# Kernel tuning notes

Hardware: AMD Instinct MI355X
Metric: run time of the kernel (lower is better)

The kernel has to match this reference:

```python
import jax, jax.numpy as jnp
import numpy as np
import math

B, NIN, DIM, QK, GS, L, BINS = 512, 128, 512, 128, 32, 2, 100
HID = int(DIM * 2.0)
G = NIN // GS
ROT = 32  # rotary dim = min(32, query_key_dim)
EPS = 1e-5


def setup_inputs() -> dict:
    key = jax.random.key(0)
    ks = jax.random.split(key, 8)
    r = jax.random.normal
    return {
        "tokens": jax.random.randint(ks[0], (B, NIN), 0, BINS),
        "emb": r(ks[1], (NIN, BINS, DIM), jnp.float32) * 0.02,
        "pos_emb": r(ks[2], (NIN, DIM), jnp.float32) * 0.01,
        "norm_g": jnp.ones((L,), jnp.float32),
        "Wh": r(ks[3], (L, DIM, 2 * HID), jnp.float32) / math.sqrt(DIM),
        "bh": jnp.zeros((L, 2 * HID), jnp.float32),
        "Wqk": r(ks[4], (L, DIM, QK), jnp.float32) / math.sqrt(DIM),
        "bqk": jnp.zeros((L, QK), jnp.float32),
        "gamma": r(ks[5], (L, 4, QK), jnp.float32) * 0.02,
        "beta": jnp.zeros((L, 4, QK), jnp.float32),
        "rp": r(ks[6], (L, 32), jnp.float32) * 0.02,
        "Wout": r(ks[7], (L, HID, DIM), jnp.float32) / math.sqrt(HID),
        "bout": jnp.zeros((L, DIM), jnp.float32),
        "ln_g": jnp.ones((DIM,), jnp.float32),
        "ln_b": jnp.zeros((DIM,), jnp.float32),
    }


def _t5_buckets(n, num_buckets=32, max_distance=128):
    # causal T5 relative position buckets, computed statically
    pos = np.arange(n)
    rel = pos[None, :] - pos[:, None]
    neg = np.maximum(-rel, 0)
    max_exact = num_buckets // 2
    vl = max_exact + (np.log(np.maximum(neg, 1) / max_exact) / np.log(max_distance / max_exact) * (num_buckets - max_exact)).astype(np.int64)
    vl = np.minimum(vl, num_buckets - 1)
    return jnp.asarray(np.where(neg < max_exact, neg, vl))


def _rotary_cos_sin(n):
    inv = 1.0 / (10000.0 ** (np.arange(0, ROT, 2) / ROT))
    f = np.einsum('i,j->ij', np.arange(n), inv)  # [n, ROT/2]
    f = np.repeat(f, 2, axis=-1)                 # interleaved-pair freqs [n, ROT]
    return jnp.asarray(np.cos(f), jnp.float32), jnp.asarray(np.sin(f), jnp.float32)


def _apply_rotary(x, cos, sin):
    xr, xp = x[..., :ROT], x[..., ROT:]
    x2 = xr.reshape(*xr.shape[:-1], ROT // 2, 2)
    rh = jnp.stack((-x2[..., 1], x2[..., 0]), axis=-1).reshape(xr.shape)
    return jnp.concatenate([xr * cos + rh * sin, xp], axis=-1)


def reference(tokens, emb, pos_emb, norm_g, Wh, bh, Wqk, bqk, gamma, beta, rp, Wout, bout, ln_g, ln_b):
    # per-column embedding lookup + positional embedding
    x = emb[jnp.arange(NIN)[None, :], tokens] + pos_emb  # [B, NIN, DIM]
    buckets = _t5_buckets(GS)
    cos, sin = _rotary_cos_sin(NIN)
    t5_scale = QK ** 0.5
    causal_mask = jnp.triu(jnp.ones((GS, GS), bool), 1)

    def grp(t):
        return t.reshape(B, G, GS, t.shape[-1])

    def layer(h, p):
        ng, Wh_l, bh_l, Wqk_l, bqk_l, gm, bt, rp_l, Wo_l, bo_l = p
        # ScaleNorm
        nrm = jnp.linalg.norm(h, axis=-1, keepdims=True) * DIM ** -0.5
        nx = h / jnp.maximum(nrm, EPS) * ng
        # shift_tokens: shift first half of features by one position
        xs, xp = nx[..., :DIM // 2], nx[..., DIM // 2:]
        xs = jnp.pad(xs, ((0, 0), (1, 0), (0, 0)))[:, :-1]
        nx = jnp.concatenate([xs, xp], axis=-1)
        hid = jax.nn.silu(nx @ Wh_l + bh_l)
        v, gate = hid[..., :HID], hid[..., HID:]
        qk = jax.nn.silu(nx @ Wqk_l + bqk_l)
        qs = qk[..., None, :] * gm + bt  # [B, NIN, 4, QK]
        quad_q = _apply_rotary(qs[..., 0, :], cos, sin)
        lin_q = _apply_rotary(qs[..., 1, :], cos, sin)
        quad_k = _apply_rotary(qs[..., 2, :], cos, sin)
        lin_k = _apply_rotary(qs[..., 3, :], cos, sin)
        qq, lq, kk, lk, vg = map(grp, (quad_q, lin_q, quad_k, lin_k, v))
        # grouped quadratic attention with ReLU^2 attn fn and T5 rel-pos bias
        sim = jnp.einsum('bgid,bgjd->bgij', qq, kk) / GS + rp_l[buckets] * t5_scale
        attn = jnp.square(jax.nn.relu(sim))
        attn = jnp.where(causal_mask, 0.0, attn)
        quad_out = jnp.einsum('bgij,bgje->bgie', attn, vg)
        # causal linear attention across groups (shifted cumsum of kv stats)
        lin_kv = jnp.einsum('bgnd,bgne->bgde', lk, vg) / GS
        lin_kv = jnp.cumsum(lin_kv, axis=1)
        lin_kv = jnp.pad(lin_kv, ((0, 0), (1, 0), (0, 0), (0, 0)))[:, :-1]
        lin_out = jnp.einsum('bgde,bgnd->bgne', lin_kv, lq)
        out = gate * (quad_out + lin_out).reshape(B, NIN, HID)
        return out @ Wo_l + bo_l + h, None

    x, _ = jax.lax.scan(layer, x, (norm_g, Wh, bh, Wqk, bqk, gamma, beta, rp, Wout, bout))
    mu = x.mean(-1, keepdims=True)
    var = x.var(-1, keepdims=True)
    return (x - mu) / jnp.sqrt(var + EPS) * ln_g + ln_b
```

## Files before the change

### kernel.cpp

```cpp
#include <hip/hip_runtime.h>
#include <hip/hip_bf16.h>
#include <math.h>
#include <stdint.h>

#define BB   512
#define NIN  128
#define DIMD 512
#define QKD  128
#define GSZ  32
#define GRP  4
#define HID  1024
#define HID2 2048
#define NFUSE 2176
#define ROT  32
#define NLAYER 2
#define EPSF 1e-5f
#define BINS 100

typedef __bf16 bf16x8 __attribute__((ext_vector_type(8)));
typedef float  f32x4  __attribute__((ext_vector_type(4)));
typedef float  f32x16 __attribute__((ext_vector_type(16)));

__device__ __forceinline__ unsigned short f2bf(float f) {
    union { float f; uint32_t u; } v; v.f = f;
    return (unsigned short)((v.u + 0x7FFFu + ((v.u >> 16) & 1u)) >> 16);
}
__device__ __forceinline__ float bf2f(unsigned short h) {
    union { uint32_t u; float f; } v; v.u = ((uint32_t)h) << 16;
    return v.f;
}

__global__ void k_embed(const int* __restrict__ tokens, const float* __restrict__ emb,
                        const float* __restrict__ pos, float* __restrict__ h) {
    int bn = blockIdx.x;
    int n  = bn % NIN;
    int tok = tokens[bn];
    const float4* e4 = (const float4*)(emb + ((size_t)n * BINS + tok) * DIMD);
    const float4* p4 = (const float4*)(pos + (size_t)n * DIMD);
    float4* h4 = (float4*)(h + (size_t)bn * DIMD);
    int t = threadIdx.x;
    float4 a = e4[t], b = p4[t];
    h4[t] = make_float4(a.x + b.x, a.y + b.y, a.z + b.z, a.w + b.w);
}

__global__ void k_rms(const float* __restrict__ h, float* __restrict__ scale,
                      const float* __restrict__ ngp) {
    int row  = blockIdx.x * 4 + (threadIdx.x >> 6);
    int lane = threadIdx.x & 63;
    const float4* r4 = (const float4*)(h + (size_t)row * DIMD);
    float s = 0.f;
    #pragma unroll
    for (int i = 0; i < 2; ++i) {
        float4 v = r4[lane + 64 * i];
        s += v.x * v.x + v.y * v.y + v.z * v.z + v.w * v.w;
    }
    #pragma unroll
    for (int o = 32; o; o >>= 1) s += __shfl_down(s, o);
    if (lane == 0) {
        float nrm = sqrtf(s) * (1.0f / sqrtf((float)DIMD));
        scale[row] = ngp[0] / fmaxf(nrm, EPSF);
    }
}

__global__ void k_nx(const float* __restrict__ h, const float* __restrict__ scale,
                     unsigned short* __restrict__ nx) {
    int bn = blockIdx.x; int n = bn % NIN;
    int t = threadIdx.x;
    float4 v; float sc;
    if (t < 64) {
        if (n == 0) {
            ((ushort4*)(nx + (size_t)bn * DIMD))[t] = make_ushort4(0, 0, 0, 0);
            return;
        }
        sc = scale[bn - 1];
        v = ((const float4*)(h + (size_t)(bn - 1) * DIMD))[t];
    } else {
        sc = scale[bn];
        v = ((const float4*)(h + (size_t)bn * DIMD))[t];
    }
    ushort4 o = make_ushort4(f2bf(v.x * sc), f2bf(v.y * sc), f2bf(v.z * sc), f2bf(v.w * sc));
    ((ushort4*)(nx + (size_t)bn * DIMD))[t] = o;
}

__global__ void k_wcast(const float* __restrict__ W, unsigned short* __restrict__ Wt,
                        int K, int N) {
    int idx = blockIdx.x * 256 + threadIdx.x;
    int total = N * (K / 8);
    if (idx >= total) return;
    int kb = idx / N, n = idx % N;
    #pragma unroll
    for (int j = 0; j < 8; ++j)
        Wt[(size_t)n * K + kb * 8 + j] = f2bf(W[(size_t)(kb * 8 + j) * N + n]);
}

#define GLOAD_LDS(gp, lp) __builtin_amdgcn_global_load_lds( \
    (const __attribute__((address_space(1))) uint32_t*)(gp), \
    (__attribute__((address_space(3))) uint32_t*)(lp), 16, 0, 0)

template<int MODE>
__global__ __launch_bounds__(256, 2) void k_gemm2(
        const unsigned short* __restrict__ A,
        const unsigned short* __restrict__ Bt,
        const float* __restrict__ bias0,
        const float* __restrict__ bias1,
        const float* __restrict__ resid,
        float* __restrict__ Cf,
        unsigned short* __restrict__ vTp,
        unsigned short* __restrict__ gatep,
        int M, int N, int K) {
    __shared__ unsigned short As[2][256 * 32];
    __shared__ unsigned short Bs[2][128 * 32];
    const int tid = threadIdx.x;

    int flat = blockIdx.y * gridDim.x + blockIdx.x;
    int nwg  = gridDim.x * gridDim.y;
    int q = nwg >> 3, r = nwg & 7;
    int xcd = flat & 7, idx = flat >> 3;
    int swz = (xcd < r ? xcd * (q + 1) : r * (q + 1) + (xcd - r) * q) + idx;
    const int bxi = swz % gridDim.x, byi = swz / gridDim.x;
    const int bm = byi * 256, bn = bxi * 128;

    const int lane = tid & 63, wave = tid >> 6;
    const int l15 = lane & 15, l4 = lane >> 4;

    f32x4 acc[4][8];
    #pragma unroll
    for (int i = 0; i < 4; ++i)
        #pragma unroll
        for (int j = 0; j < 8; ++j) acc[i][j] = (f32x4){0.f, 0.f, 0.f, 0.f};

    const int rowA = tid >> 2;
    const int colO = (tid & 3) * 16;
    const int colS = colO ^ ((rowA & 3) << 4);
    const char* gA = (const char*)(A  + (size_t)(bm + rowA) * K) + colS;
    const char* gB = (const char*)(Bt + (size_t)(bn + rowA) * K) + colS;
    const size_t stride64 = (size_t)64 * K * 2;
    unsigned short* dA0 = &As[0][tid * 8];
    unsigned short* dA1 = &As[1][tid * 8];
    unsigned short* dB0 = &Bs[0][tid * 8];
    unsigned short* dB1 = &Bs[1][tid * 8];

    #define STAGE2(dA, dB, k0) do { \
        const char* sA_ = gA + (size_t)(k0) * 2; \
        const char* sB_ = gB + (size_t)(k0) * 2; \
        GLOAD_LDS(sA_,                 (dA)); \
        GLOAD_LDS(sA_ +     stride64,  (dA) + 2048); \
        GLOAD_LDS(sA_ + 2 * stride64,  (dA) + 4096); \
        GLOAD_LDS(sA_ + 3 * stride64,  (dA) + 6144); \
        GLOAD_LDS(sB_,                 (dB)); \
        GLOAD_LDS(sB_ +     stride64,  (dB) + 2048); \
    } while (0)

    STAGE2(dA0, dB0, 0);
    asm volatile("s_waitcnt vmcnt(0)" ::: "memory");
    __syncthreads();

    const int NIT = K / 32;
    int bufc = 0;
    for (int it = 0; it < NIT; ++it) {
        if (it + 1 < NIT) {
            if (bufc == 0) STAGE2(dA1, dB1, (it + 1) * 32);
            else           STAGE2(dA0, dB0, (it + 1) * 32);
        }
        const unsigned short* Ab = As[bufc];
        const unsigned short* Bb = Bs[bufc];
        bf16x8 af[4], bfr[8];
        #pragma unroll
        for (int f = 0; f < 4; ++f) {
            int rA = wave * 64 + f * 16 + l15;
            af[f] = *(const bf16x8*)&Ab[rA * 32 + ((l4 ^ (rA & 3)) << 3)];
        }
        #pragma unroll
        for (int c = 0; c < 8; ++c) {
            int rB = c * 16 + l15;
            bfr[c] = *(const bf16x8*)&Bb[rB * 32 + ((l4 ^ (rB & 3)) << 3)];
        }
        #pragma unroll
        for (int f = 0; f < 4; ++f)
            #pragma unroll
            for (int c = 0; c < 8; ++c)
                acc[f][c] = __builtin_amdgcn_mfma_f32_16x16x32_bf16(af[f], bfr[c], acc[f][c], 0, 0, 0);
        asm volatile("s_waitcnt vmcnt(0)" ::: "memory");
        __syncthreads();
        bufc ^= 1;
    }
    #undef STAGE2

    #pragma unroll
    for (int f = 0; f < 4; ++f) {
        const int n0 = wave * 64 + f * 16 + l4 * 4;
        #pragma unroll
        for (int c = 0; c < 8; ++c) {
            const int col = bn + c * 16 + l15;
            if (MODE == 0) {
                float bsv = (col < 2 * HID) ? bias0[col] : bias1[col - 2 * HID];
                float vv[4];
                #pragma unroll
                for (int rr = 0; rr < 4; ++rr) {
                    float v = acc[f][c][rr] + bsv;
                    vv[rr] = v / (1.0f + __expf(-v));
                }
                if (col < HID) {
                    size_t batch = (size_t)byi * 2 + (n0 >> 7);
                    ushort4 o = make_ushort4(f2bf(vv[0]), f2bf(vv[1]), f2bf(vv[2]), f2bf(vv[3]));
                    *(ushort4*)&vTp[(batch * HID + col) * NIN + (n0 & 127)] = o;
                } else if (col < 2 * HID) {
                    #pragma unroll
                    for (int rr = 0; rr < 4; ++rr)
                        gatep[(size_t)(bm + n0 + rr) * HID + (col - HID)] = f2bf(vv[rr]);
                } else {
                    #pragma unroll
                    for (int rr = 0; rr < 4; ++rr)
                        Cf[(size_t)(bm + n0 + rr) * QKD + (col - 2 * HID)] = vv[rr];
                }
            } else {
                float bsv = bias0[col];
                #pragma unroll
                for (int rr = 0; rr < 4; ++rr) {
                    size_t row = bm + n0 + rr;
                    Cf[row * N + col] = acc[f][c][rr] + bsv + resid[row * N + col];
                }
            }
        }
    }
}

__global__ void k_cossin(float* __restrict__ cosb, float* __restrict__ sinb) {
    int idx = blockIdx.x * 256 + threadIdx.x;
    if (idx >= NIN * 16) return;
    int n = idx / 16, i = idx % 16;
    double inv = pow(10000.0, -(double)(2 * i) / (double)ROT);
    double f = (double)n * inv;
    cosb[idx] = (float)cos(f);
    sinb[idx] = (float)sin(f);
}

__global__ void k_rot(const float* __restrict__ qk, const float* __restrict__ gm,
                      const float* __restrict__ bt, const float* __restrict__ cosb,
                      const float* __restrict__ sinb, unsigned short* __restrict__ q4) {
    int bn = blockIdx.x; int n = bn % NIN;
    int d = threadIdx.x;
    float x = qk[(size_t)bn * QKD + d];
    float xp0 = 0.f;
    int dp = d ^ 1;
    if (d < ROT) xp0 = qk[(size_t)bn * QKD + dp];
    #pragma unroll
    for (int c = 0; c < 4; ++c) {
        float val = x * gm[c * QKD + d] + bt[c * QKD + d];
        float outv;
        if (d < ROT) {
            int i = d >> 1;
            float cs = cosb[n * 16 + i], sn = sinb[n * 16 + i];
            float xp = xp0 * gm[c * QKD + dp] + bt[c * QKD + dp];
            outv = ((d & 1) == 0) ? (val * cs - xp * sn) : (val * cs + xp * sn);
        } else outv = val;
        q4[((size_t)bn * 4 + c) * QKD + d] = f2bf(outv);
    }
}

__global__ __launch_bounds__(256) void k_attn2(
        const unsigned short* __restrict__ q4,
        const unsigned short* __restrict__ gatep,
        const unsigned short* __restrict__ vT,
        const float* __restrict__ rp,
        unsigned short* __restrict__ attn_out) {
    int et = blockIdx.x, b = blockIdx.y;
    int tid = threadIdx.x, wave = tid >> 6, lane = tid & 63;
    int l31 = lane & 31, lhi = lane >> 5;

    __shared__ unsigned short S[32][136];
    __shared__ float rps_d[32];
    if (tid < 32) {
        int d = tid, bucket;
        if (d < 16) bucket = d;
        else {
            bucket = 16 + (int)(logf((float)d * (1.0f / 16.0f)) * (16.0f / logf(8.0f)));
            if (bucket > 31) bucket = 31;
        }
        rps_d[tid] = rp[bucket] * sqrtf((float)QKD);
    }
    __syncthreads();

    size_t bbase = (size_t)b * NIN;
    int e0 = et * 256 + wave * 64;
    const unsigned short* vbase = vT + (size_t)b * HID * NIN;

    for (int g = 0; g < GRP; ++g) {
        if (wave <= g) {
            int gp = wave;
            bool quad = (gp == g);
            const unsigned short* Qb = q4 + ((bbase + g  * 32 + l31) * 4 + (quad ? 0 : 1)) * QKD;
            const unsigned short* Kb = q4 + ((bbase + gp * 32 + l31) * 4 + (quad ? 2 : 3)) * QKD;
            f32x16 sa = {};
            #pragma unroll
            for (int kk = 0; kk < 8; ++kk) {
                bf16x8 aq = *(const bf16x8*)(Qb + kk * 16 + lhi * 8);
                bf16x8 bk = *(const bf16x8*)(Kb + kk * 16 + lhi * 8);
                sa = __builtin_amdgcn_mfma_f32_32x32x16_bf16(aq, bk, sa, 0, 0, 0);
            }
            int j = l31;
            #pragma unroll
            for (int r = 0; r < 16; ++r) {
                int i = (r & 3) + 8 * (r >> 2) + 4 * lhi;
                float s = sa[r] * (1.0f / GSZ);
                if (quad) {
                    if (j > i) s = 0.f;
                    else {
                        s += rps_d[i - j];
                        s = fmaxf(s, 0.f);
                        s = s * s;
                    }
                }
                S[i][gp * 32 + j] = f2bf(s);
            }
        }
        __syncthreads();

        f32x16 o0 = {}, o1 = {};
        int KT = 2 * (g + 1);
        for (int kk = 0; kk < KT; ++kk) {
            int k0 = kk * 16 + lhi * 8;
            bf16x8 af = *(const bf16x8*)&S[l31][k0];
            bf16x8 b0 = *(const bf16x8*)(vbase + (size_t)(e0 + l31) * NIN + k0);
            bf16x8 b1 = *(const bf16x8*)(vbase + (size_t)(e0 + 32 + l31) * NIN + k0);
            o0 = __builtin_amdgcn_mfma_f32_32x32x16_bf16(af, b0, o0, 0, 0, 0);
            o1 = __builtin_amdgcn_mfma_f32_32x32x16_bf16(af, b1, o1, 0, 0, 0);
        }
        __syncthreads();

        int ea = e0 + l31, eb = e0 + 32 + l31;
        #pragma unroll
        for (int r = 0; r < 16; ++r) {
            int i = (r & 3) + 8 * (r >> 2) + 4 * lhi;
            size_t row = bbase + g * 32 + i;
            float ga = bf2f(gatep[row * HID + ea]);
            float gb = bf2f(gatep[row * HID + eb]);
            attn_out[row * HID + ea] = f2bf(ga * o0[r]);
            attn_out[row * HID + eb] = f2bf(gb * o1[r]);
        }
    }
}

__global__ void k_ln(const float* __restrict__ h, const float* __restrict__ lng,
                     const float* __restrict__ lnb, float* __restrict__ out) {
    int bn = blockIdx.x;
    int t = threadIdx.x;
    const float4* r4 = (const float4*)(h + (size_t)bn * DIMD);
    float4 v = r4[t];
    float s  = v.x + v.y + v.z + v.w;
    float sq = v.x * v.x + v.y * v.y + v.z * v.z + v.w * v.w;
    __shared__ float red[4];
    #pragma unroll
    for (int o = 32; o; o >>= 1) { s += __shfl_down(s, o); sq += __shfl_down(sq, o); }
    int lane = t & 63, w = t >> 6;
    if (lane == 0) { red[w] = s; red[2 + w] = sq; }
    __syncthreads();
    float mu  = (red[0] + red[1]) * (1.0f / DIMD);
    float var = (red[2] + red[3]) * (1.0f / DIMD) - mu * mu;
    float rstd = 1.0f / sqrtf(var + EPSF);
    float4 gg = ((const float4*)lng)[t];
    float4 bb = ((const float4*)lnb)[t];
    float4 o;
    o.x = (v.x - mu) * rstd * gg.x + bb.x;
    o.y = (v.y - mu) * rstd * gg.y + bb.y;
    o.z = (v.z - mu) * rstd * gg.z + bb.z;
    o.w = (v.w - mu) * rstd * gg.w + bb.w;
    ((float4*)(out + (size_t)bn * DIMD))[t] = o;
}

extern "C" void kernel_launch(void* const* d_in, const int* in_sizes, int n_in,
                              void* d_out, int out_size, void* d_ws, size_t ws_size,
                              hipStream_t stream) {
    const int*   tokens = (const int*)d_in[0];
    const float* emb    = (const float*)d_in[1];
    const float* pos    = (const float*)d_in[2];
    const float* norm_g = (const float*)d_in[3];
    const float* Wh     = (const float*)d_in[4];
    const float* bh     = (const float*)d_in[5];
    const float* Wqk    = (const float*)d_in[6];
    const float* bqk    = (const float*)d_in[7];
    const float* gamma  = (const float*)d_in[8];
    const float* beta   = (const float*)d_in[9];
    const float* rp     = (const float*)d_in[10];
    const float* Wout   = (const float*)d_in[11];
    const float* bout   = (const float*)d_in[12];
    const float* lng    = (const float*)d_in[13];
    const float* lnb    = (const float*)d_in[14];

    float* h  = (float*)d_out;
    float* ws = (float*)d_ws;

    size_t off = 0;
    float* scale = ws + off; off += (size_t)BB * NIN;
    float* cosb  = ws + off; off += NIN * 16;
    float* sinb  = ws + off; off += NIN * 16;
    unsigned short* whqkT = (unsigned short*)(ws + off); off += (size_t)NLAYER * NFUSE * DIMD / 2;
    unsigned short* woutT = (unsigned short*)(ws + off); off += (size_t)NLAYER * DIMD * HID / 2;
    off = (off + 63) & ~(size_t)63;
    const size_t fixedFloats = off;

    const size_t wsFloats = ws_size / sizeof(float);
    const size_t perBatch = (size_t)NIN * (DIMD / 2 + HID / 2 + HID / 2 + QKD + DIMD / 2 + HID / 2);
    int CB = BB;
    while (CB > 2 && fixedFloats + (size_t)CB * perBatch + 64 > wsFloats) CB >>= 1;

    unsigned short* nx    = (unsigned short*)(ws + off); off += (size_t)CB * NIN * DIMD / 2;
    unsigned short* vT    = (unsigned short*)(ws + off); off += (size_t)CB * HID * NIN / 2;
    unsigned short* gateB = (unsigned short*)(ws + off); off += (size_t)CB * NIN * HID / 2;
    float*          qk    = ws + off;                    off += (size_t)CB * NIN * QKD;
    unsigned short* q4    = (unsigned short*)(ws + off); off += (size_t)CB * NIN * DIMD / 2;
    unsigned short* attnB = (unsigned short*)(ws + off); off += (size_t)CB * NIN * HID / 2;

    const int BN_ = BB * NIN;

    k_cossin<<<8, 256, 0, stream>>>(cosb, sinb);
    k_embed<<<BN_, 128, 0, stream>>>(tokens, emb, pos, h);

    for (int l = 0; l < NLAYER; ++l) {
        unsigned short* whqkT_l = whqkT + (size_t)l * NFUSE * DIMD;
        k_wcast<<<(HID2 * DIMD / 8 + 255) / 256, 256, 0, stream>>>(
            Wh + (size_t)l * DIMD * HID2,  whqkT_l, DIMD, HID2);
        k_wcast<<<(QKD * DIMD / 8 + 255) / 256, 256, 0, stream>>>(
            Wqk + (size_t)l * DIMD * QKD,  whqkT_l + (size_t)HID2 * DIMD, DIMD, QKD);
        k_wcast<<<(DIMD * HID / 8 + 255) / 256, 256, 0, stream>>>(
            Wout + (size_t)l * HID * DIMD, woutT + (size_t)l * DIMD * HID, HID, DIMD);
    }

    for (int l = 0; l < NLAYER; ++l) {
        const float* bh_l  = bh   + (size_t)l * HID2;
        const float* bqk_l = bqk  + (size_t)l * QKD;
        const float* gm_l  = gamma+ (size_t)l * 4 * QKD;
        const float* bt_l  = beta + (size_t)l * 4 * QKD;
        const float* rp_l  = rp   + (size_t)l * 32;
        const float* bo_l  = bout + (size_t)l * DIMD;
        const unsigned short* whqkT_l = whqkT + (size_t)l * NFUSE * DIMD;
        const unsigned short* woutT_l = woutT + (size_t)l * DIMD * HID;

        for (int c0 = 0; c0 < BB; c0 += CB) {
            const int rowsC = CB * NIN;
            float* h_c = h + (size_t)c0 * NIN * DIMD;

            k_rms<<<rowsC / 4, 256, 0, stream>>>(h_c, scale, norm_g + l);
            k_nx<<<rowsC, 128, 0, stream>>>(h_c, scale, nx);

            dim3 g1(NFUSE / 128, rowsC / 256);
            k_gemm2<0><<<g1, 256, 0, stream>>>(nx, whqkT_l, bh_l, bqk_l, nullptr,
                                               qk, vT, gateB, rowsC, NFUSE, DIMD);

            k_rot<<<rowsC, 128, 0, stream>>>(qk, gm_l, bt_l, cosb, sinb, q4);

            dim3 ga(HID / 256, CB);
            k_attn2<<<ga, 256, 0, stream>>>(q4, gateB, vT, rp_l, attnB);

            dim3 g3(DIMD / 128, rowsC / 256);
            k_gemm2<1><<<g3, 256, 0, stream>>>(attnB, woutT_l, bo_l, nullptr, h_c,
                                               h_c, nullptr, nullptr, rowsC, DIMD, HID);
        }
    }

    k_ln<<<BN_, 128, 0, stream>>>(h, lng, lnb, (float*)d_out);
}
```

Before: 1.429 ms.

## Fuse RMS norm with shift-cast and retile fused projection GEMM to 128x128

Merges the RMS-scale kernel and the token-shift/bf16-cast kernel into one. Each block now reduces its own row and writes the shifted half to the next row, so the separate scale buffer and one launch go away. The fused Wh/Wqk GEMM becomes its own kernel with 128x128 tiles, a 2x2 wave layout and single-buffered LDS, which doubles the grid size for better occupancy and load balance. The new GEMM drops the double-buffered prefetch, so memory latency may be exposed.

```diff
diff --git a/kernel.cpp b/kernel.cpp
--- a/kernel.cpp
+++ b/kernel.cpp
@@ -43,43 +43,30 @@
     h4[t] = make_float4(a.x + b.x, a.y + b.y, a.z + b.z, a.w + b.w);
 }
 
-__global__ void k_rms(const float* __restrict__ h, float* __restrict__ scale,
+__global__ void k_nxf(const float* __restrict__ h, unsigned short* __restrict__ nx,
                       const float* __restrict__ ngp) {
-    int row  = blockIdx.x * 4 + (threadIdx.x >> 6);
-    int lane = threadIdx.x & 63;
-    const float4* r4 = (const float4*)(h + (size_t)row * DIMD);
-    float s = 0.f;
-    #pragma unroll
-    for (int i = 0; i < 2; ++i) {
-        float4 v = r4[lane + 64 * i];
-        s += v.x * v.x + v.y * v.y + v.z * v.z + v.w * v.w;
-    }
-    #pragma unroll
-    for (int o = 32; o; o >>= 1) s += __shfl_down(s, o);
-    if (lane == 0) {
-        float nrm = sqrtf(s) * (1.0f / sqrtf((float)DIMD));
-        scale[row] = ngp[0] / fmaxf(nrm, EPSF);
-    }
-}
-
-__global__ void k_nx(const float* __restrict__ h, const float* __restrict__ scale,
-                     unsigned short* __restrict__ nx) {
     int bn = blockIdx.x; int n = bn % NIN;
     int t = threadIdx.x;
-    float4 v; float sc;
+    float4 v = ((const float4*)(h + (size_t)bn * DIMD))[t];
+    float sq = v.x * v.x + v.y * v.y + v.z * v.z + v.w * v.w;
+    __shared__ float red[2];
+    #pragma unroll
+    for (int o = 32; o; o >>= 1) sq += __shfl_down(sq, o);
+    int lane = t & 63, w = t >> 6;
+    if (lane == 0) red[w] = sq;
+    __syncthreads();
+    float s = red[0] + red[1];
+    float nrm = sqrtf(s) * (1.0f / sqrtf((float)DIMD));
+    float sc = ngp[0] / fmaxf(nrm, EPSF);
+    ushort4 o = make_ushort4(f2bf(v.x * sc), f2bf(v.y * sc), f2bf(v.z * sc), f2bf(v.w * sc));
     if (t < 64) {
-        if (n == 0) {
+        if (n == 0)
             ((ushort4*)(nx + (size_t)bn * DIMD))[t] = make_ushort4(0, 0, 0, 0);
-            return;
-        }
-        sc = scale[bn - 1];
-        v = ((const float4*)(h + (size_t)(bn - 1) * DIMD))[t];
+        if (n != NIN - 1)
+            ((ushort4*)(nx + (size_t)(bn + 1) * DIMD))[t] = o;
     } else {
-        sc = scale[bn];
-        v = ((const float4*)(h + (size_t)bn * DIMD))[t];
-    }
-    ushort4 o = make_ushort4(f2bf(v.x * sc), f2bf(v.y * sc), f2bf(v.z * sc), f2bf(v.w * sc));
-    ((ushort4*)(nx + (size_t)bn * DIMD))[t] = o;
+        ((ushort4*)(nx + (size_t)bn * DIMD))[t] = o;
+    }
 }
 
 __global__ void k_wcast(const float* __restrict__ W, unsigned short* __restrict__ Wt,
@@ -97,16 +84,105 @@
     (const __attribute__((address_space(1))) uint32_t*)(gp), \
     (__attribute__((address_space(3))) uint32_t*)(lp), 16, 0, 0)
 
-template<int MODE>
-__global__ __launch_bounds__(256, 2) void k_gemm2(
+__global__ __launch_bounds__(256) void k_gemm_f(
         const unsigned short* __restrict__ A,
         const unsigned short* __restrict__ Bt,
         const float* __restrict__ bias0,
         const float* __restrict__ bias1,
-        const float* __restrict__ resid,
         float* __restrict__ Cf,
         unsigned short* __restrict__ vTp,
         unsigned short* __restrict__ gatep,
+        int M, int N, int K) {
+    __shared__ unsigned short As[128 * 32];
+    __shared__ unsigned short Bs[128 * 32];
+    const int tid = threadIdx.x;
+
+    int flat = blockIdx.y * gridDim.x + blockIdx.x;
+    int nwg  = gridDim.x * gridDim.y;
+    int q = nwg >> 3, r = nwg & 7;
+    int xcd = flat & 7, idx = flat >> 3;
+    int swz = (xcd < r ? xcd * (q + 1) : r * (q + 1) + (xcd - r) * q) + idx;
+    const int bxi = swz % gridDim.x, byi = swz / gridDim.x;
+    const int bm = byi * 128, bn = bxi * 128;
+
+    const int lane = tid & 63, wave = tid >> 6;
+    const int wm = (wave >> 1) * 64, wn = (wave & 1) * 64;
+    const int l15 = lane & 15, l4 = lane >> 4;
+
+    f32x4 acc[4][4];
+    #pragma unroll
+    for (int i = 0; i < 4; ++i)
+        #pragma unroll
+        for (int j = 0; j < 4; ++j) acc[i][j] = (f32x4){0.f, 0.f, 0.f, 0.f};
+
+    const int rowA = tid >> 2;
+    const int colO = (tid & 3) * 16;
+    const int colS = colO ^ ((rowA & 3) << 4);
+    const char* gA = (const char*)(A  + (size_t)(bm + rowA) * K) + colS;
+    const char* gB = (const char*)(Bt + (size_t)(bn + rowA) * K) + colS;
+    const size_t stride64 = (size_t)64 * K * 2;
+    unsigned short* ldsA = As + tid * 8;
+    unsigned short* ldsB = Bs + tid * 8;
+
+    for (int k0 = 0; k0 < K; k0 += 32) {
+        GLOAD_LDS(gA + (size_t)k0 * 2,            ldsA);
+        GLOAD_LDS(gA + (size_t)k0 * 2 + stride64, ldsA + 2048);
+        GLOAD_LDS(gB + (size_t)k0 * 2,            ldsB);
+        GLOAD_LDS(gB + (size_t)k0 * 2 + stride64, ldsB + 2048);
+        asm volatile("s_waitcnt vmcnt(0)" ::: "memory");
+        __syncthreads();
+
+        bf16x8 af[4], bfr[4];
+        #pragma unroll
+        for (int f = 0; f < 4; ++f) {
+            int rA = wm + f * 16 + l15;
+            int rB = wn + f * 16 + l15;
+            af[f]  = *(const bf16x8*)&As[rA * 32 + ((l4 ^ (rA & 3)) << 3)];
+            bfr[f] = *(const bf16x8*)&Bs[rB * 32 + ((l4 ^ (rB & 3)) << 3)];
+        }
+        #pragma unroll
+        for (int i = 0; i < 4; ++i)
+            #pragma unroll
+            for (int j = 0; j < 4; ++j)
+                acc[i][j] = __builtin_amdgcn_mfma_f32_16x16x32_bf16(af[i], bfr[j], acc[i][j], 0, 0, 0);
+        __syncthreads();
+    }
+
+    #pragma unroll
+    for (int i = 0; i < 4; ++i) {
+        const int n0 = wm + i * 16 + l4 * 4;
+        #pragma unroll
+        for (int j = 0; j < 4; ++j) {
+            const int col = bn + wn + j * 16 + l15;
+            float bsv = (col < 2 * HID) ? bias0[col] : bias1[col - 2 * HID];
+            float vv[4];
+            #pragma unroll
+            for (int rr = 0; rr < 4; ++rr) {
+                float v = acc[i][j][rr] + bsv;
+                vv[rr] = v / (1.0f + __expf(-v));
+            }
+            if (col < HID) {
+                ushort4 o = make_ushort4(f2bf(vv[0]), f2bf(vv[1]), f2bf(vv[2]), f2bf(vv[3]));
+                *(ushort4*)&vTp[((size_t)byi * HID + col) * NIN + n0] = o;
+            } else if (col < 2 * HID) {
+                #pragma unroll
+                for (int rr = 0; rr < 4; ++rr)
+                    gatep[(size_t)(bm + n0 + rr) * HID + (col - HID)] = f2bf(vv[rr]);
+            } else {
+                #pragma unroll
+                for (int rr = 0; rr < 4; ++rr)
+                    Cf[(size_t)(bm + n0 + rr) * QKD + (col - 2 * HID)] = vv[rr];
+            }
+        }
+    }
+}
+
+__global__ __launch_bounds__(256, 2) void k_gemm_o(
+        const unsigned short* __restrict__ A,
+        const unsigned short* __restrict__ Bt,
+        const float* __restrict__ bias0,
+        const float* __restrict__ resid,
+        float* __restrict__ Cf,
         int M, int N, int K) {
     __shared__ unsigned short As[2][256 * 32];
     __shared__ unsigned short Bs[2][128 * 32];
@@ -192,34 +268,11 @@
         #pragma unroll
         for (int c = 0; c < 8; ++c) {
             const int col = bn + c * 16 + l15;
-            if (MODE == 0) {
-                float bsv = (col < 2 * HID) ? bias0[col] : bias1[col - 2 * HID];
-                float vv[4];
-                #pragma unroll
-                for (int rr = 0; rr < 4; ++rr) {
-                    float v = acc[f][c][rr] + bsv;
-                    vv[rr] = v / (1.0f + __expf(-v));
-                }
-                if (col < HID) {
-                    size_t batch = (size_t)byi * 2 + (n0 >> 7);
-                    ushort4 o = make_ushort4(f2bf(vv[0]), f2bf(vv[1]), f2bf(vv[2]), f2bf(vv[3]));
-                    *(ushort4*)&vTp[(batch * HID + col) * NIN + (n0 & 127)] = o;
-                } else if (col < 2 * HID) {
-                    #pragma unroll
-                    for (int rr = 0; rr < 4; ++rr)
-                        gatep[(size_t)(bm + n0 + rr) * HID + (col - HID)] = f2bf(vv[rr]);
-                } else {
-                    #pragma unroll
-                    for (int rr = 0; rr < 4; ++rr)
-                        Cf[(size_t)(bm + n0 + rr) * QKD + (col - 2 * HID)] = vv[rr];
-                }
-            } else {
-                float bsv = bias0[col];
-                #pragma unroll
-                for (int rr = 0; rr < 4; ++rr) {
-                    size_t row = bm + n0 + rr;
-                    Cf[row * N + col] = acc[f][c][rr] + bsv + resid[row * N + col];
-                }
+            float bsv = bias0[col];
+            #pragma unroll
+            for (int rr = 0; rr < 4; ++rr) {
+                size_t row = bm + n0 + rr;
+                Cf[row * N + col] = acc[f][c][rr] + bsv + resid[row * N + col];
             }
         }
     }
@@ -391,7 +444,6 @@
     float* ws = (float*)d_ws;
 
     size_t off = 0;
-    float* scale = ws + off; off += (size_t)BB * NIN;
     float* cosb  = ws + off; off += NIN * 16;
     float* sinb  = ws + off; off += NIN * 16;
     unsigned short* whqkT = (unsigned short*)(ws + off); off += (size_t)NLAYER * NFUSE * DIMD / 2;
@@ -440,12 +492,11 @@
             const int rowsC = CB * NIN;
             float* h_c = h + (size_t)c0 * NIN * DIMD;
 
-            k_rms<<<rowsC / 4, 256, 0, stream>>>(h_c, scale, norm_g + l);
-            k_nx<<<rowsC, 128, 0, stream>>>(h_c, scale, nx);
-
-            dim3 g1(NFUSE / 128, rowsC / 256);
-            k_gemm2<0><<<g1, 256, 0, stream>>>(nx, whqkT_l, bh_l, bqk_l, nullptr,
-                                               qk, vT, gateB, rowsC, NFUSE, DIMD);
+            k_nxf<<<rowsC, 128, 0, stream>>>(h_c, nx, norm_g + l);
+
+            dim3 g1(NFUSE / 128, rowsC / 128);
+            k_gemm_f<<<g1, 256, 0, stream>>>(nx, whqkT_l, bh_l, bqk_l,
+                                             qk, vT, gateB, rowsC, NFUSE, DIMD);
 
             k_rot<<<rowsC, 128, 0, stream>>>(qk, gm_l, bt_l, cosb, sinb, q4);
 
@@ -453,8 +504,8 @@
             k_attn2<<<ga, 256, 0, stream>>>(q4, gateB, vT, rp_l, attnB);
 
             dim3 g3(DIMD / 128, rowsC / 256);
-            k_gemm2<1><<<g3, 256, 0, stream>>>(attnB, woutT_l, bo_l, nullptr, h_c,
-                                               h_c, nullptr, nullptr, rowsC, DIMD, HID);
+            k_gemm_o<<<g3, 256, 0, stream>>>(attnB, woutT_l, bo_l, h_c, h_c,
+                                             rowsC, DIMD, HID);
         }
     }
 
```

New measurement: 1.383 ms. 3.2% less time.
